# Optimization experiments

Hardware: AMD Instinct MI355X
Metric: run time of the kernel (lower is better)

Reference implementation:

```python
import jax, jax.numpy as jnp
import numpy as np

D_MIN, D_MAX, D_COUNT = 0.0, 20.0, 16  # RBF basis as in _rbf
EPS = 1e-6


def _rbf(d):
    # d: [...] -> [..., 16]
    mu = jnp.linspace(D_MIN, D_MAX, D_COUNT)
    sigma = (D_MAX - D_MIN) / D_COUNT
    return jnp.exp(-(((d[..., None] - mu) / sigma) ** 2))


def setup_inputs() -> dict:
    key = jax.random.key(0)
    k1, k2, k3 = jax.random.split(key, 3)
    N = 32768
    X = jax.random.normal(k1, (N, 4, 3), dtype=jnp.float32) * 10.0
    segment_ids = jax.random.randint(k2, (N,), 0, 3, dtype=jnp.int32)
    is_global = jax.random.randint(k3, (N,), 0, 2, dtype=jnp.int32).astype(bool)
    return {"X": X, "segment_ids": segment_ids, "is_global": is_global,
            "batch_size": 16, "top_k": 9}


def reference(X, segment_ids, is_global, batch_size, top_k):
    N = X.shape[0]
    B = batch_size
    L = N // B
    K = top_k

    # ---- per-batch dense pairwise distance + KNN (vectorized _knn_edges) ----
    Xca = X[:, 1, :].reshape(B, L, 3)                      # CA atoms per chain
    dX = Xca[:, :, None, :] - Xca[:, None, :, :]            # [B, L, L, 3]
    D = jnp.sqrt(jnp.sum(dX * dX, axis=-1) + EPS)           # [B, L, L]
    _, E_idx = jax.lax.top_k(-D, K)                         # smallest-K -> [B, L, K]

    offs = (jnp.arange(B, dtype=E_idx.dtype) * L)[:, None, None]
    col = (E_idx + offs).reshape(-1)                        # [N*K] global col idx
    row = jnp.repeat(jnp.arange(N, dtype=col.dtype), K)     # [N*K]

    row_seg, col_seg = segment_ids[row], segment_ids[col]
    not_global = jnp.logical_not(is_global[row] | is_global[col])
    ctx_mask = (row_seg == col_seg) & not_global            # ctx (intra-segment) edges
    inter_mask = (row_seg != col_seg) & not_global          # inter-segment edges

    # ---- node distance RBF features (get_node_dist) ----
    def node_d(i):
        return jnp.sqrt(jnp.sum((X[:, i, :] - X[:, 1, :]) ** 2, axis=1) + EPS)
    dis_node_feats = jnp.concatenate(
        [_rbf(node_d(0)), _rbf(node_d(2)), _rbf(node_d(3))], axis=1)  # [N, 48]

    # ---- edge distance RBF features on KNN edges (get_edge_dist) ----
    X_row, X_col = X[row], X[col]                           # [N*K, 4, 3]
    def edge_d(i):
        return jnp.sqrt(jnp.sum((X_row[:, i, :] - X_col[:, 1, :]) ** 2, axis=1) + EPS)
    dis_edge_feats = jnp.concatenate(
        [_rbf(edge_d(0)), _rbf(edge_d(1)), _rbf(edge_d(2)), _rbf(edge_d(3))],
        axis=1)                                             # [N*K, 64]

    return dis_node_feats, dis_edge_feats, row, col, ctx_mask, inter_mask
```

## Files before the change

kernel.cpp:

```cpp
#include <hip/hip_runtime.h>
#include <cstdint>
#include <cstddef>

#define NN   32768
#define BATCH 16
#define LL   2048
#define KNN  9
#define NE   (NN * KNN)
#define PLM  5
#define MTOP 12
#define RPW  2
#define TPB  1024
#define ROWS_PB ((TPB / 64) * RPW)


__device__ __forceinline__ float ref_d2(float ax, float ay, float az,
                                        float bx, float by, float bz) {
    float dx = __fsub_rn(ax, bx);
    float dy = __fsub_rn(ay, by);
    float dz = __fsub_rn(az, bz);
    return __fadd_rn(__fadd_rn(__fmul_rn(dx, dx), __fmul_rn(dy, dy)),
                     __fmul_rn(dz, dz));
}

__device__ __forceinline__ float ref_dist(float ax, float ay, float az,
                                          float bx, float by, float bz) {
    return sqrtf(__fadd_rn(ref_d2(ax, ay, az, bx, by, bz), 1e-6f));
}

__device__ __forceinline__ unsigned dpp_min16_4(unsigned x) {
    unsigned t;
    t = (unsigned)__builtin_amdgcn_update_dpp((int)0xFFFFFFFF, (int)x, 0x111, 0xf, 0xf, false);
    x = min(x, t);
    t = (unsigned)__builtin_amdgcn_update_dpp((int)0xFFFFFFFF, (int)x, 0x112, 0xf, 0xf, false);
    x = min(x, t);
    t = (unsigned)__builtin_amdgcn_update_dpp((int)0xFFFFFFFF, (int)x, 0x114, 0xf, 0xf, false);
    x = min(x, t);
    t = (unsigned)__builtin_amdgcn_update_dpp((int)0xFFFFFFFF, (int)x, 0x118, 0xf, 0xf, false);
    x = min(x, t);
    return x;
}

__device__ __forceinline__ unsigned gather_min(unsigned a) {
    unsigned m0 = min((unsigned)__builtin_amdgcn_readlane((int)a, 15),
                      (unsigned)__builtin_amdgcn_readlane((int)a, 31));
    unsigned m1 = min((unsigned)__builtin_amdgcn_readlane((int)a, 47),
                      (unsigned)__builtin_amdgcn_readlane((int)a, 63));
    return min(m0, m1);
}

__global__ __launch_bounds__(TPB, 8) void fused_kernel(
    const float* __restrict__ X, const int* __restrict__ seg,
    const int* __restrict__ isg_raw,
    float* __restrict__ node_out, float* __restrict__ edge_out,
    float* __restrict__ out_row, float* __restrict__ out_col,
    float* __restrict__ out_ctx, float* __restrict__ out_inter)
{
    __shared__ float4 crd[LL];
    __shared__ float rowatoms[ROWS_PB * 12];
    __shared__ unsigned char code[LL];
    __shared__ int colsL[TPB / 64][RPW][KNN];
    __shared__ int flag;

    int tid  = threadIdx.x;
    int row0 = blockIdx.x * ROWS_PB;
    int base = row0 & ~(LL - 1);

    if (tid == 0) flag = 0;
    __syncthreads();
    if (tid < 512) {
        unsigned v = (unsigned)isg_raw[(base >> 2) + tid];
        if (v > 1u) atomicOr(&flag, 1);
    }
    if (tid < ROWS_PB * 12)
        rowatoms[tid] = X[(size_t)row0 * 12 + tid];
    __syncthreads();
    bool as_bytes = (flag != 0);
    for (int t = tid; t < LL; t += TPB) {
        const float* p = X + (size_t)(base + t) * 12 + 3;
        float x = p[0], y = p[1], z = p[2];
        crd[t] = make_float4(x, y, z, fmaf(x, x, fmaf(y, y, z * z)));
        int ig = as_bytes ? (int)((const unsigned char*)isg_raw)[base + t]
                          : isg_raw[base + t];
        code[t] = (unsigned char)((seg[base + t] & 3) | (ig ? 4 : 0));
    }
    __syncthreads();

    int lane = tid & 63;
    int warp = tid >> 6;
    int gi0  = row0 + warp * RPW;
    int i0   = gi0 - base;

    float qx[RPW], qy[RPW], qz[RPW], qn[RPW];
#pragma unroll
    for (int r = 0; r < RPW; ++r) {
        float4 ci = crd[i0 + r];
        qx[r] = ci.x; qy[r] = ci.y; qz[r] = ci.z; qn[r] = ci.w;
    }

    unsigned lst[RPW][PLM];
#pragma unroll
    for (int r = 0; r < RPW; ++r)
#pragma unroll
        for (int k = 0; k < PLM; ++k) lst[r][k] = 0xFFFFFFFFu;

#pragma unroll 4
    for (int s = 0; s < LL / 64; ++s) {
        int j = (s << 6) | lane;
        float4 c = crd[j];
#pragma unroll
        for (int r = 0; r < RPW; ++r) {
            float dot = fmaf(qx[r], c.x, fmaf(qy[r], c.y, qz[r] * c.z));
            float d2  = fmaf(-2.0f, dot, qn[r] + c.w);
            unsigned cur = (__float_as_uint(d2) & 0xFFFFF800u) | (unsigned)j;
#pragma unroll
            for (int k = 0; k < PLM; ++k) {
                unsigned lo = min(lst[r][k], cur);
                cur = max(lst[r][k], cur);
                lst[r][k] = lo;
            }
        }
    }

    unsigned mine[RPW];
#pragma unroll
    for (int r = 0; r < RPW; ++r) mine[r] = 0xFFFFFFFFu;

#pragma unroll
    for (int t = 0; t < MTOP; ++t) {
        unsigned a0 = dpp_min16_4(lst[0][0]);
        unsigned a1 = dpp_min16_4(lst[1][0]);
        unsigned m0 = gather_min(a0);
        unsigned m1 = gather_min(a1);
        bool rem0 = (lst[0][0] == m0);
        bool rem1 = (lst[1][0] == m1);
#pragma unroll
        for (int k = 0; k < PLM - 1; ++k) {
            lst[0][k] = rem0 ? lst[0][k + 1] : lst[0][k];
            lst[1][k] = rem1 ? lst[1][k + 1] : lst[1][k];
        }
        lst[0][PLM - 1] = rem0 ? 0xFFFFFFFFu : lst[0][PLM - 1];
        lst[1][PLM - 1] = rem1 ? 0xFFFFFFFFu : lst[1][PLM - 1];
        mine[0] = (lane == t) ? m0 : mine[0];
        mine[1] = (lane == t) ? m1 : mine[1];
    }

#pragma unroll
    for (int r = 0; r < RPW; ++r) {
        int gi = gi0 + r;
        int jf = (int)(mine[r] & (LL - 1));
        float4 cj = crd[jf];
        float D = sqrtf(__fadd_rn(ref_d2(qx[r], qy[r], qz[r], cj.x, cj.y, cj.z), 1e-6f));
        int rank = 0;
#pragma unroll
        for (int t = 0; t < MTOP; ++t) {
            float Dt = __int_as_float(__builtin_amdgcn_readlane(__float_as_int(D), t));
            int   jt = __builtin_amdgcn_readlane(jf, t);
            bool lt = (Dt < D) || (Dt == D && jt < jf);
            rank += lt ? 1 : 0;
        }
        if (lane < MTOP && rank < KNN) {
            int cg = base + jf;
            int e  = gi * KNN + rank;
            out_row[e] = (float)gi;
            out_col[e] = (float)cg;
            int cr = code[gi - base], cc = code[jf];
            int ng = ((cr | cc) & 4) ? 0 : 1;
            int sr = cr & 3, sc = cc & 3;
            out_ctx[e]   = (sr == sc && ng) ? 1.0f : 0.0f;
            out_inter[e] = (sr != sc && ng) ? 1.0f : 0.0f;
            colsL[warp][r][rank] = jf;
        }
    }

    {
        int g = lane & 15, sE = lane >> 4;
        int atomE = g >> 2;
        float zk[4];
        float tbE = (float)((g & 3) * 4);
#pragma unroll
        for (int k = 0; k < 4; ++k)
            zk[k] = -(tbE + (float)k) * (20.0f / 15.0f) * 0.8f;
        int rA = warp * RPW;
        if (sE < 3) {
#pragma unroll
            for (int p = 0; p < 3 * RPW; ++p) {
                int r = p / 3;
                int q = (p % 3) * 3 + sE;
                int jf = colsL[warp][r][q];
                float4 cj = crd[jf];
                const float* ra = &rowatoms[(rA + r) * 12 + atomE * 3];
                float d = ref_dist(ra[0], ra[1], ra[2], cj.x, cj.y, cj.z);
                float4 v;
                float z0 = fmaf(d, 0.8f, zk[0]); v.x = __expf(-z0 * z0);
                float z1 = fmaf(d, 0.8f, zk[1]); v.y = __expf(-z1 * z1);
                float z2 = fmaf(d, 0.8f, zk[2]); v.z = __expf(-z2 * z2);
                float z3 = fmaf(d, 0.8f, zk[3]); v.w = __expf(-z3 * z3);
                *(float4*)(edge_out + ((size_t)(gi0 + r) * KNN + q) * 64 + g * 4) = v;
            }
        }
    }

    if (lane < 24) {
        int rn = lane / 12;
        int c4 = lane - rn * 12;
        int aN = c4 >> 2;
        int asrc = (aN == 0) ? 0 : aN + 1;
        float tbN = (float)((c4 & 3) * 4);
        float zn[4];
#pragma unroll
        for (int k = 0; k < 4; ++k)
            zn[k] = -(tbN + (float)k) * (20.0f / 15.0f) * 0.8f;
        const float* ra = &rowatoms[(warp * RPW + rn) * 12 + asrc * 3];
        float4 ca = crd[i0 + rn];
        float d = ref_dist(ra[0], ra[1], ra[2], ca.x, ca.y, ca.z);
        float4 v;
        float z0 = fmaf(d, 0.8f, zn[0]); v.x = __expf(-z0 * z0);
        float z1 = fmaf(d, 0.8f, zn[1]); v.y = __expf(-z1 * z1);
        float z2 = fmaf(d, 0.8f, zn[2]); v.z = __expf(-z2 * z2);
        float z3 = fmaf(d, 0.8f, zn[3]); v.w = __expf(-z3 * z3);
        *(float4*)(node_out + (size_t)(gi0 + rn) * 48 + c4 * 4) = v;
    }
}

extern "C" void kernel_launch(void* const* d_in, const int* in_sizes, int n_in,
                              void* d_out, int out_size, void* d_ws, size_t ws_size,
                              hipStream_t stream) {
    const float* X       = (const float*)d_in[0];
    const int*   seg     = (const int*)d_in[1];
    const int*   isg_raw = (const int*)d_in[2];

    float* out = (float*)d_out;
    float* node_out  = out;
    float* edge_out  = out + (size_t)NN * 48;
    float* row_out   = edge_out + (size_t)NE * 64;
    float* col_out   = row_out + NE;
    float* ctx_out   = col_out + NE;
    float* inter_out = ctx_out + NE;

    hipLaunchKernelGGL(fused_kernel, dim3(NN / ROWS_PB), dim3(TPB), 0, stream,
                       X, seg, isg_raw,
                       node_out, edge_out, row_out, col_out, ctx_out, inter_out);
}
```

Baseline: 60.74 us.

## Process four rows per wavefront and fold -2 factor into query coordinates

Raises the number of query rows each wavefront handles from two to four, so each coordinate loaded from LDS during the candidate scan is reused across more rows. The top-k merge loop is generalised over RPW, and the node-feature lanes are widened to cover the extra rows. The distance expression pre-scales the query by -2 to save one FMA, and clamps the result at zero before it is turned into a sort key. The cost is more registers per thread (4x5 candidate lists), which may lower occupancy or cause spills at 1024 threads per block, and the grid is half as large.

```diff
diff --git a/kernel.cpp b/kernel.cpp
--- a/kernel.cpp
+++ b/kernel.cpp
@@ -9,7 +9,7 @@
 #define NE   (NN * KNN)
 #define PLM  5
 #define MTOP 12
-#define RPW  2
+#define RPW  4
 #define TPB  1024
 #define ROWS_PB ((TPB / 64) * RPW)
 
@@ -91,11 +91,12 @@
     int gi0  = row0 + warp * RPW;
     int i0   = gi0 - base;
 
-    float qx[RPW], qy[RPW], qz[RPW], qn[RPW];
+    float qx2[RPW], qy2[RPW], qz2[RPW], qn[RPW];
 #pragma unroll
     for (int r = 0; r < RPW; ++r) {
         float4 ci = crd[i0 + r];
-        qx[r] = ci.x; qy[r] = ci.y; qz[r] = ci.z; qn[r] = ci.w;
+        qx2[r] = -2.0f * ci.x; qy2[r] = -2.0f * ci.y; qz2[r] = -2.0f * ci.z;
+        qn[r] = ci.w;
     }
 
     unsigned lst[RPW][PLM];
@@ -104,14 +105,16 @@
 #pragma unroll
         for (int k = 0; k < PLM; ++k) lst[r][k] = 0xFFFFFFFFu;
 
-#pragma unroll 4
+#pragma unroll 8
     for (int s = 0; s < LL / 64; ++s) {
         int j = (s << 6) | lane;
         float4 c = crd[j];
 #pragma unroll
         for (int r = 0; r < RPW; ++r) {
-            float dot = fmaf(qx[r], c.x, fmaf(qy[r], c.y, qz[r] * c.z));
-            float d2  = fmaf(-2.0f, dot, qn[r] + c.w);
+            float d2 = fmaf(qx2[r], c.x,
+                       fmaf(qy2[r], c.y,
+                       fmaf(qz2[r], c.z, qn[r] + c.w)));
+            d2 = fmaxf(d2, 0.0f);
             unsigned cur = (__float_as_uint(d2) & 0xFFFFF800u) | (unsigned)j;
 #pragma unroll
             for (int k = 0; k < PLM; ++k) {
@@ -128,29 +131,28 @@
 
 #pragma unroll
     for (int t = 0; t < MTOP; ++t) {
-        unsigned a0 = dpp_min16_4(lst[0][0]);
-        unsigned a1 = dpp_min16_4(lst[1][0]);
-        unsigned m0 = gather_min(a0);
-        unsigned m1 = gather_min(a1);
-        bool rem0 = (lst[0][0] == m0);
-        bool rem1 = (lst[1][0] == m1);
-#pragma unroll
-        for (int k = 0; k < PLM - 1; ++k) {
-            lst[0][k] = rem0 ? lst[0][k + 1] : lst[0][k];
-            lst[1][k] = rem1 ? lst[1][k + 1] : lst[1][k];
-        }
-        lst[0][PLM - 1] = rem0 ? 0xFFFFFFFFu : lst[0][PLM - 1];
-        lst[1][PLM - 1] = rem1 ? 0xFFFFFFFFu : lst[1][PLM - 1];
-        mine[0] = (lane == t) ? m0 : mine[0];
-        mine[1] = (lane == t) ? m1 : mine[1];
+        unsigned a[RPW], m[RPW];
+#pragma unroll
+        for (int r = 0; r < RPW; ++r) a[r] = dpp_min16_4(lst[r][0]);
+#pragma unroll
+        for (int r = 0; r < RPW; ++r) m[r] = gather_min(a[r]);
+#pragma unroll
+        for (int r = 0; r < RPW; ++r) {
+            bool rem = (lst[r][0] == m[r]);
+#pragma unroll
+            for (int k = 0; k < PLM - 1; ++k) lst[r][k] = rem ? lst[r][k + 1] : lst[r][k];
+            lst[r][PLM - 1] = rem ? 0xFFFFFFFFu : lst[r][PLM - 1];
+            mine[r] = (lane == t) ? m[r] : mine[r];
+        }
     }
 
 #pragma unroll
     for (int r = 0; r < RPW; ++r) {
         int gi = gi0 + r;
+        float4 ci = crd[i0 + r];
         int jf = (int)(mine[r] & (LL - 1));
         float4 cj = crd[jf];
-        float D = sqrtf(__fadd_rn(ref_d2(qx[r], qy[r], qz[r], cj.x, cj.y, cj.z), 1e-6f));
+        float D = sqrtf(__fadd_rn(ref_d2(ci.x, ci.y, ci.z, cj.x, cj.y, cj.z), 1e-6f));
         int rank = 0;
 #pragma unroll
         for (int t = 0; t < MTOP; ++t) {
@@ -201,7 +203,7 @@
         }
     }
 
-    if (lane < 24) {
+    if (lane < 48) {
         int rn = lane / 12;
         int c4 = lane - rn * 12;
         int aN = c4 >> 2;
```

Measured after the change: 58.24 us. -4.1%, faster.
